# Performance work log

Hardware: AMD Instinct MI355X
Metric: run time of the kernel (lower is better)

Reference implementation:

```python
import jax, jax.numpy as jnp
import numpy as np

DIM = 256
HEADS = 8
WIN = 7          # window height/width
N = WIN * WIN    # tokens per window
HEAD_DIM = DIM // HEADS
CPB_HIDDEN = 512


def _relative_coords_table():
    # [1, 2W-1, 2W-1, 2] log-spaced continuous coords (Swin-V2 CPB input)
    rh = np.arange(-(WIN - 1), WIN, dtype=np.float32)
    rw = np.arange(-(WIN - 1), WIN, dtype=np.float32)
    hh, ww = np.meshgrid(rh, rw, indexing='ij')
    table = np.stack([hh, ww], axis=-1)[None]  # [1, 13, 13, 2]
    table[..., 0] /= (WIN - 1)
    table[..., 1] /= (WIN - 1)
    table *= 8.0
    table = np.sign(table) * np.log(np.abs(table) + 1.0) / np.log(8.0)
    return jnp.asarray(table, dtype=jnp.float32)


def _relative_position_index():
    ch = np.arange(WIN)
    cw = np.arange(WIN)
    coords = np.stack(np.meshgrid(ch, cw, indexing='ij'))  # [2, W, W]
    flat = coords.reshape(2, -1)                            # [2, N]
    rel = flat[:, :, None] - flat[:, None, :]               # [2, N, N]
    rel = rel.transpose(1, 2, 0)
    rel[..., 0] += WIN - 1
    rel[..., 1] += WIN - 1
    rel[..., 0] *= 2 * WIN - 1
    return jnp.asarray(rel.sum(-1), dtype=jnp.int32)        # [N, N]


def setup_inputs() -> dict:
    key = jax.random.key(0)
    ks = jax.random.split(key, 9)
    B = 2048
    s_in = 1.0 / np.sqrt(DIM)
    s_cpb1 = 1.0 / np.sqrt(2.0)
    s_cpb2 = 1.0 / np.sqrt(CPB_HIDDEN)
    return {
        "x": jax.random.normal(ks[0], (B, N, DIM), dtype=jnp.float32),
        "qkv_w": jax.random.normal(ks[1], (DIM, 3 * DIM), dtype=jnp.float32) * s_in,
        "qkv_b": jnp.zeros((3 * DIM,), dtype=jnp.float32),
        "proj_w": jax.random.normal(ks[2], (DIM, DIM), dtype=jnp.float32) * s_in,
        "proj_b": jnp.zeros((DIM,), dtype=jnp.float32),
        "logit_scale": jnp.full((HEADS, 1, 1), np.log(10.0), dtype=jnp.float32),
        "cpb_w1": jax.random.normal(ks[3], (2, CPB_HIDDEN), dtype=jnp.float32) * s_cpb1,
        "cpb_b1": jnp.zeros((CPB_HIDDEN,), dtype=jnp.float32),
        "cpb_w2": jax.random.normal(ks[4], (CPB_HIDDEN, HEADS), dtype=jnp.float32) * s_cpb2,
    }


def reference(x, qkv_w, qkv_b, proj_w, proj_b, logit_scale, cpb_w1, cpb_b1, cpb_w2):
    B = x.shape[0]
    coords_table = _relative_coords_table()       # [1, 13, 13, 2]
    rel_pos_index = _relative_position_index()    # [N, N]

    # QKV projection -> [3, B, H, N, D]
    qkv = (x @ qkv_w + qkv_b).reshape(B, N, 3, HEADS, HEAD_DIM)
    qkv = jnp.transpose(qkv, (2, 0, 3, 1, 4))
    q, k, v = qkv[0], qkv[1], qkv[2]

    # cosine attention: L2-normalize q and k
    qn = q / jnp.linalg.norm(q, axis=-1, keepdims=True)
    kn = k / jnp.linalg.norm(k, axis=-1, keepdims=True)
    attn = jnp.einsum('bhnd,bhmd->bhnm', qn, kn)

    scale = jnp.exp(jnp.clip(logit_scale, -100.0, np.log(1.0 / 0.01)))  # [H,1,1]
    attn = attn * scale[None]

    # CPB-MLP relative position bias
    h = jax.nn.gelu(coords_table @ cpb_w1 + cpb_b1, approximate=False)
    bias_table = (h @ cpb_w2).reshape(-1, HEADS)              # [(2W-1)^2, H]
    bias = bias_table[rel_pos_index.reshape(-1)]              # [N*N, H]
    bias = bias.reshape(N, N, HEADS).transpose(2, 0, 1)       # [H, N, N]
    bias = 16.0 * jax.nn.sigmoid(bias)
    attn = attn + bias[None]

    attn = jax.nn.softmax(attn, axis=-1)

    out = jnp.einsum('bhnm,bhmd->bhnd', attn, v)
    out = jnp.transpose(out, (0, 2, 1, 3)).reshape(B, N, DIM)
    return out @ proj_w + proj_b
```

## Files before the change

kernel.cpp:

```cpp
#include <hip/hip_runtime.h>

typedef _Float16 f16;
typedef _Float16 f16x4 __attribute__((ext_vector_type(4)));
typedef _Float16 f16x8 __attribute__((ext_vector_type(8)));
typedef float f32x4 __attribute__((ext_vector_type(4)));

#define WS_BIAS    0
#define WS_TBL     131072
#define WS_QKVWT   136704
#define WS_PROJWT  529920
#define WS_ATTNOUT 660992

__global__ __launch_bounds__(512) void cpb_mlp_kernel(
    const float* __restrict__ w1, const float* __restrict__ b1,
    const float* __restrict__ w2, float* __restrict__ tbl)
{
    const int bid = blockIdx.x;
    const int i = bid / 13, j = bid % 13;
    float t0 = 8.0f * (float)(i - 6) / 6.0f;
    float t1 = 8.0f * (float)(j - 6) / 6.0f;
    const float invlog8 = 0.4808983469629878f;
    t0 = copysignf(log1pf(fabsf(t0)) * invlog8, t0);
    t1 = copysignf(log1pf(fabsf(t1)) * invlog8, t1);

    const int t = threadIdx.x;
    float pre = t0 * w1[t] + t1 * w1[512 + t] + b1[t];
    float g = 0.5f * pre * (1.0f + erff(pre * 0.70710678118654752f));
    float a[8];
#pragma unroll
    for (int h = 0; h < 8; ++h) a[h] = g * w2[t * 8 + h];
#pragma unroll
    for (int off = 1; off < 64; off <<= 1)
#pragma unroll
        for (int h = 0; h < 8; ++h) a[h] += __shfl_xor(a[h], off, 64);

    __shared__ float wred[8][8];
    const int w = t >> 6, lane = t & 63;
    if (lane == 0)
#pragma unroll
        for (int h = 0; h < 8; ++h) wred[w][h] = a[h];
    __syncthreads();
    if (t < 8) {
        float s = 0.f;
#pragma unroll
        for (int ww = 0; ww < 8; ++ww) s += wred[ww][t];
        tbl[bid * 8 + t] = s;
    }
}

__global__ __launch_bounds__(256) void cpb_bias_kernel(
    const float* __restrict__ tbl, float* __restrict__ bias_ws)
{
    int idx = blockIdx.x * 256 + threadIdx.x;
    int h = idx >> 12, r = (idx >> 6) & 63, c = idx & 63;
    float v = 0.f;
    if (r < 49 && c < 49) {
        int dh = r / 7 - c / 7 + 6;
        int dw = r % 7 - c % 7 + 6;
        float bv = tbl[(dh * 13 + dw) * 8 + h];
        v = 16.0f / (1.0f + __expf(-bv));
    }
    bias_ws[idx] = v;
}

__global__ __launch_bounds__(256) void wconv_kernel(
    const float* __restrict__ qkv_w, const float* __restrict__ proj_w,
    f16* __restrict__ qkv_wT, f16* __restrict__ proj_wT)
{
    __shared__ float ts[64][65];
    int b = blockIdx.x;
    const float* src; f16* dst; int W, kb, nb;
    if (b < 48) { src = qkv_w;  dst = qkv_wT;  W = 768; kb = b / 12; nb = b % 12; }
    else { b -= 48; src = proj_w; dst = proj_wT; W = 256; kb = b / 4;  nb = b % 4; }
    const int t = threadIdx.x;
#pragma unroll
    for (int it = 0; it < 4; ++it) {
        int k = it * 16 + (t >> 4);
        int n4 = (t & 15) * 4;
        float4 v = *(const float4*)(src + (size_t)(kb * 64 + k) * W + nb * 64 + n4);
        ts[k][n4] = v.x; ts[k][n4 + 1] = v.y; ts[k][n4 + 2] = v.z; ts[k][n4 + 3] = v.w;
    }
    __syncthreads();
#pragma unroll
    for (int it = 0; it < 4; ++it) {
        int n = it * 16 + (t >> 4);
        int k4 = (t & 15) * 4;
        f16x4 hv;
        hv[0] = (f16)ts[k4][n]; hv[1] = (f16)ts[k4 + 1][n];
        hv[2] = (f16)ts[k4 + 2][n]; hv[3] = (f16)ts[k4 + 3][n];
        *(f16x4*)(dst + (size_t)(nb * 64 + n) * 256 + kb * 64 + k4) = hv;
    }
}

__global__ __launch_bounds__(256, 3) void win_attn_kernel(
    const float* __restrict__ x, const float* __restrict__ qkv_b,
    const float* __restrict__ logit_scale, const f16* __restrict__ qkv_wT,
    const float* __restrict__ bias_ws, f16* __restrict__ attn_out, int nwg)
{
    __shared__ alignas(16) char smem0[18432];
    __shared__ alignas(16) f16 qs[2][64][40];
    __shared__ alignas(16) f16 kq[2][64][40];
    __shared__ alignas(16) f16 vT[2][32][72];
    __shared__ float invq_s[2][64];
    __shared__ float invk_s[2][64];
    f16 (*xs)[136] = reinterpret_cast<f16(*)[136]>(smem0);
    f16 (*ps)[72]  = reinterpret_cast<f16(*)[72]>(smem0);

    const int orig = blockIdx.x;
    const int wg = ((nwg & 7) == 0) ? ((orig & 7) * (nwg >> 3) + (orig >> 3)) : orig;
    const int b  = wg >> 2;
    const int hp = wg & 3;

    const int tid = threadIdx.x;
    const int lane = tid & 63;
    const int w = tid >> 6;
    const int l15 = lane & 15, lq = lane >> 4;
    const int hl = w >> 1;
    const int dh = w & 1;
    const int head = hp * 2 + hl;

    const float* xb = x + (size_t)b * (49 * 256);
    const int srow = tid >> 5;
    const int scol = (tid & 31) * 4;

    float4 sreg[8];
#pragma unroll
    for (int i = 0; i < 8; ++i) {
        int r = i * 8 + srow;
        sreg[i] = (r < 49) ? *(const float4*)(xb + r * 256 + scol) : make_float4(0.f, 0.f, 0.f, 0.f);
    }
#pragma unroll
    for (int i = 0; i < 8; ++i) {
        int r = i * 8 + srow;
        f16x4 hv; hv[0] = (f16)sreg[i].x; hv[1] = (f16)sreg[i].y; hv[2] = (f16)sreg[i].z; hv[3] = (f16)sreg[i].w;
        *(f16x4*)(&xs[r][scol]) = hv;
    }
    __syncthreads();

#pragma unroll
    for (int i = 0; i < 8; ++i) {
        int r = i * 8 + srow;
        sreg[i] = (r < 49) ? *(const float4*)(xb + r * 256 + 128 + scol) : make_float4(0.f, 0.f, 0.f, 0.f);
    }

    f32x4 acc[3][4];
#pragma unroll
    for (int ci = 0; ci < 3; ++ci)
#pragma unroll
        for (int mt = 0; mt < 4; ++mt) { acc[ci][mt][0] = 0.f; acc[ci][mt][1] = 0.f; acc[ci][mt][2] = 0.f; acc[ci][mt][3] = 0.f; }

    const int bcol = head * 32 + dh * 16 + l15;

#pragma unroll
    for (int ks = 0; ks < 4; ++ks) {
        f16x8 af[4];
#pragma unroll
        for (int mt = 0; mt < 4; ++mt) af[mt] = *(const f16x8*)(&xs[mt * 16 + l15][ks * 32 + lq * 8]);
#pragma unroll
        for (int ci = 0; ci < 3; ++ci) {
            f16x8 bf = *(const f16x8*)(qkv_wT + (size_t)(ci * 256 + bcol) * 256 + ks * 32 + lq * 8);
#pragma unroll
            for (int mt = 0; mt < 4; ++mt)
                acc[ci][mt] = __builtin_amdgcn_mfma_f32_16x16x32_f16(af[mt], bf, acc[ci][mt], 0, 0, 0);
        }
    }
    __syncthreads();

#pragma unroll
    for (int i = 0; i < 8; ++i) {
        int r = i * 8 + srow;
        f16x4 hv; hv[0] = (f16)sreg[i].x; hv[1] = (f16)sreg[i].y; hv[2] = (f16)sreg[i].z; hv[3] = (f16)sreg[i].w;
        *(f16x4*)(&xs[r][scol]) = hv;
    }
    __syncthreads();

#pragma unroll
    for (int ks = 0; ks < 4; ++ks) {
        f16x8 af[4];
#pragma unroll
        for (int mt = 0; mt < 4; ++mt) af[mt] = *(const f16x8*)(&xs[mt * 16 + l15][ks * 32 + lq * 8]);
#pragma unroll
        for (int ci = 0; ci < 3; ++ci) {
            f16x8 bf = *(const f16x8*)(qkv_wT + (size_t)(ci * 256 + bcol) * 256 + 128 + ks * 32 + lq * 8);
#pragma unroll
            for (int mt = 0; mt < 4; ++mt)
                acc[ci][mt] = __builtin_amdgcn_mfma_f32_16x16x32_f16(af[mt], bf, acc[ci][mt], 0, 0, 0);
        }
    }

    {
        float bq = qkv_b[bcol], bk = qkv_b[256 + bcol], bv = qkv_b[512 + bcol];
        const int d = dh * 16 + l15;
#pragma unroll
        for (int mt = 0; mt < 4; ++mt)
#pragma unroll
            for (int j = 0; j < 4; ++j) {
                int row = mt * 16 + lq * 4 + j;
                qs[hl][row][d] = (f16)(acc[0][mt][j] + bq);
                kq[hl][row][d] = (f16)(acc[1][mt][j] + bk);
                vT[hl][d][row] = (f16)(acc[2][mt][j] + bv);
            }
    }
    __syncthreads();

    {
        const int isK = tid >> 7;
        const int h2 = (tid >> 6) & 1;
        const int row = tid & 63;
        const f16* rp = isK ? &kq[h2][row][0] : &qs[h2][row][0];
        float ss = 0.f;
#pragma unroll
        for (int c8 = 0; c8 < 4; ++c8) {
            f16x8 v = *(const f16x8*)(rp + c8 * 8);
#pragma unroll
            for (int e = 0; e < 8; ++e) { float f = (float)v[e]; ss += f * f; }
        }
        float inv = rsqrtf(fmaxf(ss, 1e-20f));
        if (isK) invk_s[h2][row] = inv;
        else {
            float sc = __expf(fminf(logit_scale[hp * 2 + h2], 4.605170185988091f));
            invq_s[h2][row] = inv * sc;
        }
    }
    __syncthreads();

    const int mh = w & 1;
    f32x4 sacc[2][4];
#pragma unroll
    for (int a = 0; a < 2; ++a)
#pragma unroll
        for (int c = 0; c < 4; ++c) { sacc[a][c][0] = 0.f; sacc[a][c][1] = 0.f; sacc[a][c][2] = 0.f; sacc[a][c][3] = 0.f; }
#pragma unroll
    for (int mtl = 0; mtl < 2; ++mtl) {
        int mt = mh * 2 + mtl;
        f16x8 qf = *(const f16x8*)(&qs[hl][mt * 16 + l15][lq * 8]);
#pragma unroll
        for (int nt = 0; nt < 4; ++nt) {
            f16x8 kf = *(const f16x8*)(&kq[hl][nt * 16 + l15][lq * 8]);
            sacc[mtl][nt] = __builtin_amdgcn_mfma_f32_16x16x32_f16(qf, kf, sacc[mtl][nt], 0, 0, 0);
        }
    }

    const float* biash = bias_ws + head * 4096;
#pragma unroll
    for (int mtl = 0; mtl < 2; ++mtl) {
#pragma unroll
        for (int j = 0; j < 4; ++j) {
            int row = (mh * 2 + mtl) * 16 + lq * 4 + j;
            float iq = invq_s[hl][row];
            float tv[4];
#pragma unroll
            for (int nt = 0; nt < 4; ++nt) {
                int col = nt * 16 + l15;
                float sv = sacc[mtl][nt][j] * iq * invk_s[hl][col] + biash[row * 64 + col];
                tv[nt] = (col < 49) ? sv : -1e30f;
            }
            float mx = fmaxf(fmaxf(tv[0], tv[1]), fmaxf(tv[2], tv[3]));
#pragma unroll
            for (int off = 1; off < 16; off <<= 1) mx = fmaxf(mx, __shfl_xor(mx, off, 64));
            float p[4], sum = 0.f;
#pragma unroll
            for (int nt = 0; nt < 4; ++nt) { p[nt] = __expf(tv[nt] - mx); sum += p[nt]; }
#pragma unroll
            for (int off = 1; off < 16; off <<= 1) sum += __shfl_xor(sum, off, 64);
            float invsum = 1.0f / sum;
#pragma unroll
            for (int nt = 0; nt < 4; ++nt) ps[hl * 64 + row][nt * 16 + l15] = (f16)(p[nt] * invsum);
        }
    }

    f32x4 oacc[2][2];
#pragma unroll
    for (int a = 0; a < 2; ++a)
#pragma unroll
        for (int c = 0; c < 2; ++c) { oacc[a][c][0] = 0.f; oacc[a][c][1] = 0.f; oacc[a][c][2] = 0.f; oacc[a][c][3] = 0.f; }
#pragma unroll
    for (int mtl = 0; mtl < 2; ++mtl) {
        int mt = mh * 2 + mtl;
#pragma unroll
        for (int kb = 0; kb < 2; ++kb) {
            f16x8 pf = *(const f16x8*)(&ps[hl * 64 + mt * 16 + l15][kb * 32 + lq * 8]);
#pragma unroll
            for (int nt = 0; nt < 2; ++nt) {
                f16x8 vf = *(const f16x8*)(&vT[hl][nt * 16 + l15][kb * 32 + lq * 8]);
                oacc[mtl][nt] = __builtin_amdgcn_mfma_f32_16x16x32_f16(pf, vf, oacc[mtl][nt], 0, 0, 0);
            }
        }
    }
#pragma unroll
    for (int mtl = 0; mtl < 2; ++mtl)
#pragma unroll
        for (int j = 0; j < 4; ++j) {
            int row = (mh * 2 + mtl) * 16 + lq * 4 + j;
            if (row < 49) {
#pragma unroll
                for (int nt = 0; nt < 2; ++nt)
                    attn_out[((size_t)(b * 49 + row)) * 256 + head * 32 + nt * 16 + l15] = (f16)oacc[mtl][nt][j];
            }
        }
}

__global__ __launch_bounds__(256, 4) void proj_kernel(
    const f16* __restrict__ attn_out, const f16* __restrict__ proj_wT,
    const float* __restrict__ proj_b, float* __restrict__ out, int Mtot)
{
    __shared__ alignas(16) f16 as[64][264];
    const int tid = threadIdx.x, lane = tid & 63, w = tid >> 6;
    const int l15 = lane & 15, lq = lane >> 4;
    const int mb = blockIdx.x;

#pragma unroll
    for (int i = 0; i < 8; ++i) {
        int r = i * 8 + (tid >> 5);
        int c = (tid & 31) * 8;
        int gr = mb * 64 + r;
        f16x8 v = {};
        if (gr < Mtot) v = *(const f16x8*)(attn_out + (size_t)gr * 256 + c);
        *(f16x8*)(&as[r][c]) = v;
    }
    __syncthreads();

    f32x4 acc[4][4];
#pragma unroll
    for (int a = 0; a < 4; ++a)
#pragma unroll
        for (int c = 0; c < 4; ++c) { acc[a][c][0] = 0.f; acc[a][c][1] = 0.f; acc[a][c][2] = 0.f; acc[a][c][3] = 0.f; }

    const f16* bbase = proj_wT + (size_t)(w * 64) * 256;
#pragma unroll
    for (int ks = 0; ks < 8; ++ks) {
        f16x8 af[4], bf[4];
#pragma unroll
        for (int mt = 0; mt < 4; ++mt) af[mt] = *(const f16x8*)(&as[mt * 16 + l15][ks * 32 + lq * 8]);
#pragma unroll
        for (int nt = 0; nt < 4; ++nt) bf[nt] = *(const f16x8*)(bbase + (size_t)(nt * 16 + l15) * 256 + ks * 32 + lq * 8);
#pragma unroll
        for (int mt = 0; mt < 4; ++mt)
#pragma unroll
            for (int nt = 0; nt < 4; ++nt)
                acc[mt][nt] = __builtin_amdgcn_mfma_f32_16x16x32_f16(af[mt], bf[nt], acc[mt][nt], 0, 0, 0);
    }
    float pb[4];
#pragma unroll
    for (int nt = 0; nt < 4; ++nt) pb[nt] = proj_b[w * 64 + nt * 16 + l15];
#pragma unroll
    for (int mt = 0; mt < 4; ++mt)
#pragma unroll
        for (int j = 0; j < 4; ++j) {
            int gr = mb * 64 + mt * 16 + lq * 4 + j;
            if (gr < Mtot) {
#pragma unroll
                for (int nt = 0; nt < 4; ++nt)
                    out[(size_t)gr * 256 + w * 64 + nt * 16 + l15] = acc[mt][nt][j] + pb[nt];
            }
        }
}

extern "C" void kernel_launch(void* const* d_in, const int* in_sizes, int n_in,
                              void* d_out, int out_size, void* d_ws, size_t ws_size,
                              hipStream_t stream) {
    const float* x           = (const float*)d_in[0];
    const float* qkv_w       = (const float*)d_in[1];
    const float* qkv_b       = (const float*)d_in[2];
    const float* proj_w      = (const float*)d_in[3];
    const float* proj_b      = (const float*)d_in[4];
    const float* logit_scale = (const float*)d_in[5];
    const float* cpb_w1      = (const float*)d_in[6];
    const float* cpb_b1      = (const float*)d_in[7];
    const float* cpb_w2      = (const float*)d_in[8];
    float* out = (float*)d_out;

    const int B = in_sizes[0] / (49 * 256);
    char* ws = (char*)d_ws;
    float* bias_ws = (float*)(ws + WS_BIAS);
    float* tbl_ws  = (float*)(ws + WS_TBL);
    f16* qkv_wT    = (f16*)(ws + WS_QKVWT);
    f16* proj_wT   = (f16*)(ws + WS_PROJWT);
    f16* attn_out  = (f16*)(ws + WS_ATTNOUT);

    hipLaunchKernelGGL(cpb_mlp_kernel, dim3(169), dim3(512), 0, stream, cpb_w1, cpb_b1, cpb_w2, tbl_ws);
    hipLaunchKernelGGL(cpb_bias_kernel, dim3(128), dim3(256), 0, stream, tbl_ws, bias_ws);
    hipLaunchKernelGGL(wconv_kernel, dim3(64), dim3(256), 0, stream, qkv_w, proj_w, qkv_wT, proj_wT);

    const int nwg = B * 4;
    hipLaunchKernelGGL(win_attn_kernel, dim3(nwg), dim3(256), 0, stream,
                       x, qkv_b, logit_scale, qkv_wT, bias_ws, attn_out, nwg);

    const int Mtot = B * 49;
    const int mblocks = (Mtot + 63) / 64;
    hipLaunchKernelGGL(proj_kernel, dim3(mblocks), dim3(256), 0, stream,
                       attn_out, proj_wT, proj_b, out, Mtot);
}
```

Baseline: 391.0 us.

## Fuse window attention and output projection into one per-window kernel

Merges the attention and projection kernels so that each 512-thread block handles one whole window with all 8 heads, one wave per head. The per-head attention output stays in LDS and feeds the projection GEMM directly, removing the fp16 intermediate round trip through global memory and one launch. The relative-position bias is stored as fp16 in a permuted layout and held in registers. Q/K norms are computed with in-register shuffles instead of a separate LDS pass, and softmax normalisation is deferred to the output. The cost is higher register and LDS pressure, with occupancy limited to two blocks per CU and fewer blocks overall.

```diff
diff --git a/kernel.cpp b/kernel.cpp
--- a/kernel.cpp
+++ b/kernel.cpp
@@ -6,10 +6,9 @@
 typedef float f32x4 __attribute__((ext_vector_type(4)));
 
 #define WS_BIAS    0
-#define WS_TBL     131072
-#define WS_QKVWT   136704
-#define WS_PROJWT  529920
-#define WS_ATTNOUT 660992
+#define WS_TBL     65536
+#define WS_QKVWT   73728
+#define WS_PROJWT  466944
 
 __global__ __launch_bounds__(512) void cpb_mlp_kernel(
     const float* __restrict__ w1, const float* __restrict__ b1,
@@ -49,7 +48,7 @@
 }
 
 __global__ __launch_bounds__(256) void cpb_bias_kernel(
-    const float* __restrict__ tbl, float* __restrict__ bias_ws)
+    const float* __restrict__ tbl, f16* __restrict__ bias_f16)
 {
     int idx = blockIdx.x * 256 + threadIdx.x;
     int h = idx >> 12, r = (idx >> 6) & 63, c = idx & 63;
@@ -60,7 +59,8 @@
         float bv = tbl[(dh * 13 + dw) * 8 + h];
         v = 16.0f / (1.0f + __expf(-bv));
     }
-    bias_ws[idx] = v;
+    int cc = (c & 15) * 4 + (c >> 4);
+    bias_f16[(h << 12) + (r << 6) + cc] = (f16)v;
 }
 
 __global__ __launch_bounds__(256) void wconv_kernel(
@@ -92,64 +92,67 @@
     }
 }
 
-__global__ __launch_bounds__(256, 3) void win_attn_kernel(
+__global__ __launch_bounds__(512, 2) void fused_kernel(
     const float* __restrict__ x, const float* __restrict__ qkv_b,
     const float* __restrict__ logit_scale, const f16* __restrict__ qkv_wT,
-    const float* __restrict__ bias_ws, f16* __restrict__ attn_out, int nwg)
+    const f16* __restrict__ bias_f16, const f16* __restrict__ proj_wT,
+    const float* __restrict__ proj_b, float* __restrict__ out)
 {
-    __shared__ alignas(16) char smem0[18432];
-    __shared__ alignas(16) f16 qs[2][64][40];
-    __shared__ alignas(16) f16 kq[2][64][40];
-    __shared__ alignas(16) f16 vT[2][32][72];
-    __shared__ float invq_s[2][64];
-    __shared__ float invk_s[2][64];
-    f16 (*xs)[136] = reinterpret_cast<f16(*)[136]>(smem0);
-    f16 (*ps)[72]  = reinterpret_cast<f16(*)[72]>(smem0);
-
-    const int orig = blockIdx.x;
-    const int wg = ((nwg & 7) == 0) ? ((orig & 7) * (nwg >> 3) + (orig >> 3)) : orig;
-    const int b  = wg >> 2;
-    const int hp = wg & 3;
+    __shared__ alignas(16) f16 xs[64][136];
+    __shared__ alignas(16) f16 slab[8 * 5120];
+    __shared__ alignas(16) f16 vt[8][32][72];
+    __shared__ float invk_s[8][64];
 
     const int tid = threadIdx.x;
     const int lane = tid & 63;
-    const int w = tid >> 6;
+    const int head = tid >> 6;
     const int l15 = lane & 15, lq = lane >> 4;
-    const int hl = w >> 1;
-    const int dh = w & 1;
-    const int head = hp * 2 + hl;
+    const int b = blockIdx.x;
+
+    f16x4 bias_r[16];
+    {
+        const f16* bh = bias_f16 + head * 4096;
+#pragma unroll
+        for (int mt = 0; mt < 4; ++mt)
+#pragma unroll
+            for (int j = 0; j < 4; ++j) {
+                int row = mt * 16 + lq * 4 + j;
+                bias_r[mt * 4 + j] = *(const f16x4*)(bh + row * 64 + l15 * 4);
+            }
+    }
+    const float lsc = __expf(fminf(logit_scale[head], 4.605170185988091f));
 
     const float* xb = x + (size_t)b * (49 * 256);
     const int srow = tid >> 5;
     const int scol = (tid & 31) * 4;
 
-    float4 sreg[8];
-#pragma unroll
-    for (int i = 0; i < 8; ++i) {
-        int r = i * 8 + srow;
+    float4 sreg[4];
+#pragma unroll
+    for (int i = 0; i < 4; ++i) {
+        int r = i * 16 + srow;
         sreg[i] = (r < 49) ? *(const float4*)(xb + r * 256 + scol) : make_float4(0.f, 0.f, 0.f, 0.f);
     }
 #pragma unroll
-    for (int i = 0; i < 8; ++i) {
-        int r = i * 8 + srow;
+    for (int i = 0; i < 4; ++i) {
+        int r = i * 16 + srow;
         f16x4 hv; hv[0] = (f16)sreg[i].x; hv[1] = (f16)sreg[i].y; hv[2] = (f16)sreg[i].z; hv[3] = (f16)sreg[i].w;
         *(f16x4*)(&xs[r][scol]) = hv;
     }
     __syncthreads();
 
 #pragma unroll
-    for (int i = 0; i < 8; ++i) {
-        int r = i * 8 + srow;
+    for (int i = 0; i < 4; ++i) {
+        int r = i * 16 + srow;
         sreg[i] = (r < 49) ? *(const float4*)(xb + r * 256 + 128 + scol) : make_float4(0.f, 0.f, 0.f, 0.f);
     }
 
-    f32x4 acc[3][4];
+    f32x4 acc[3][2][4];
 #pragma unroll
     for (int ci = 0; ci < 3; ++ci)
 #pragma unroll
-        for (int mt = 0; mt < 4; ++mt) { acc[ci][mt][0] = 0.f; acc[ci][mt][1] = 0.f; acc[ci][mt][2] = 0.f; acc[ci][mt][3] = 0.f; }
-
-    const int bcol = head * 32 + dh * 16 + l15;
+        for (int nt = 0; nt < 2; ++nt)
+#pragma unroll
+            for (int mt = 0; mt < 4; ++mt) { acc[ci][nt][mt][0]=0.f; acc[ci][nt][mt][1]=0.f; acc[ci][nt][mt][2]=0.f; acc[ci][nt][mt][3]=0.f; }
 
 #pragma unroll
     for (int ks = 0; ks < 4; ++ks) {
@@ -157,18 +160,20 @@
 #pragma unroll
         for (int mt = 0; mt < 4; ++mt) af[mt] = *(const f16x8*)(&xs[mt * 16 + l15][ks * 32 + lq * 8]);
 #pragma unroll
-        for (int ci = 0; ci < 3; ++ci) {
-            f16x8 bf = *(const f16x8*)(qkv_wT + (size_t)(ci * 256 + bcol) * 256 + ks * 32 + lq * 8);
-#pragma unroll
-            for (int mt = 0; mt < 4; ++mt)
-                acc[ci][mt] = __builtin_amdgcn_mfma_f32_16x16x32_f16(af[mt], bf, acc[ci][mt], 0, 0, 0);
-        }
-    }
-    __syncthreads();
-
-#pragma unroll
-    for (int i = 0; i < 8; ++i) {
-        int r = i * 8 + srow;
+        for (int ci = 0; ci < 3; ++ci)
+#pragma unroll
+            for (int nt = 0; nt < 2; ++nt) {
+                f16x8 bf = *(const f16x8*)(qkv_wT + (size_t)(ci * 256 + head * 32 + nt * 16 + l15) * 256 + ks * 32 + lq * 8);
+#pragma unroll
+                for (int mt = 0; mt < 4; ++mt)
+                    acc[ci][nt][mt] = __builtin_amdgcn_mfma_f32_16x16x32_f16(af[mt], bf, acc[ci][nt][mt], 0, 0, 0);
+            }
+    }
+    __syncthreads();
+
+#pragma unroll
+    for (int i = 0; i < 4; ++i) {
+        int r = i * 16 + srow;
         f16x4 hv; hv[0] = (f16)sreg[i].x; hv[1] = (f16)sreg[i].y; hv[2] = (f16)sreg[i].z; hv[3] = (f16)sreg[i].w;
         *(f16x4*)(&xs[r][scol]) = hv;
     }
@@ -180,178 +185,179 @@
 #pragma unroll
         for (int mt = 0; mt < 4; ++mt) af[mt] = *(const f16x8*)(&xs[mt * 16 + l15][ks * 32 + lq * 8]);
 #pragma unroll
-        for (int ci = 0; ci < 3; ++ci) {
-            f16x8 bf = *(const f16x8*)(qkv_wT + (size_t)(ci * 256 + bcol) * 256 + 128 + ks * 32 + lq * 8);
-#pragma unroll
-            for (int mt = 0; mt < 4; ++mt)
-                acc[ci][mt] = __builtin_amdgcn_mfma_f32_16x16x32_f16(af[mt], bf, acc[ci][mt], 0, 0, 0);
-        }
-    }
-
+        for (int ci = 0; ci < 3; ++ci)
+#pragma unroll
+            for (int nt = 0; nt < 2; ++nt) {
+                f16x8 bf = *(const f16x8*)(qkv_wT + (size_t)(ci * 256 + head * 32 + nt * 16 + l15) * 256 + 128 + ks * 32 + lq * 8);
+#pragma unroll
+                for (int mt = 0; mt < 4; ++mt)
+                    acc[ci][nt][mt] = __builtin_amdgcn_mfma_f32_16x16x32_f16(af[mt], bf, acc[ci][nt][mt], 0, 0, 0);
+            }
+    }
+
+    f16* myslab = slab + head * 5120;
+    float bq[2], bk[2], bv2[2];
+#pragma unroll
+    for (int nt = 0; nt < 2; ++nt) {
+        int c = head * 32 + nt * 16 + l15;
+        bq[nt] = qkv_b[c]; bk[nt] = qkv_b[256 + c]; bv2[nt] = qkv_b[512 + c];
+    }
+#pragma unroll
+    for (int nt = 0; nt < 2; ++nt)
+#pragma unroll
+        for (int mt = 0; mt < 4; ++mt)
+#pragma unroll
+            for (int j = 0; j < 4; ++j) {
+                int row = mt * 16 + lq * 4 + j, d = nt * 16 + l15;
+                vt[head][d][row] = (f16)(acc[2][nt][mt][j] + bv2[nt]);
+            }
+    float ssq[4][4], ssk[4][4], invq[4][4], invsum[4][4];
+#pragma unroll
+    for (int mt = 0; mt < 4; ++mt)
+#pragma unroll
+        for (int j = 0; j < 4; ++j) {
+            float sq = 0.f, sk = 0.f;
+            int row = mt * 16 + lq * 4 + j;
+#pragma unroll
+            for (int nt = 0; nt < 2; ++nt) {
+                int d = nt * 16 + l15;
+                float qv = acc[0][nt][mt][j] + bq[nt];
+                float kv = acc[1][nt][mt][j] + bk[nt];
+                myslab[row * 40 + d] = (f16)qv;
+                myslab[2560 + row * 40 + d] = (f16)kv;
+                sq += qv * qv; sk += kv * kv;
+            }
+            ssq[mt][j] = sq; ssk[mt][j] = sk;
+        }
+#pragma unroll
+    for (int off = 1; off < 16; off <<= 1)
+#pragma unroll
+        for (int mt = 0; mt < 4; ++mt)
+#pragma unroll
+            for (int j = 0; j < 4; ++j) {
+                ssq[mt][j] += __shfl_xor(ssq[mt][j], off, 16);
+                ssk[mt][j] += __shfl_xor(ssk[mt][j], off, 16);
+            }
+#pragma unroll
+    for (int mt = 0; mt < 4; ++mt)
+#pragma unroll
+        for (int j = 0; j < 4; ++j) {
+            invq[mt][j] = rsqrtf(fmaxf(ssq[mt][j], 1e-20f)) * lsc;
+            float ik = rsqrtf(fmaxf(ssk[mt][j], 1e-20f));
+            if (l15 == 0) invk_s[head][mt * 16 + lq * 4 + j] = ik;
+        }
+
+    f32x4 sacc[4][4];
+#pragma unroll
+    for (int a = 0; a < 4; ++a)
+#pragma unroll
+        for (int c = 0; c < 4; ++c) { sacc[a][c][0]=0.f; sacc[a][c][1]=0.f; sacc[a][c][2]=0.f; sacc[a][c][3]=0.f; }
     {
-        float bq = qkv_b[bcol], bk = qkv_b[256 + bcol], bv = qkv_b[512 + bcol];
-        const int d = dh * 16 + l15;
+        f16x8 qf[4], kf[4];
+#pragma unroll
+        for (int mt = 0; mt < 4; ++mt) qf[mt] = *(const f16x8*)(myslab + (mt * 16 + l15) * 40 + lq * 8);
+#pragma unroll
+        for (int nt = 0; nt < 4; ++nt) kf[nt] = *(const f16x8*)(myslab + 2560 + (nt * 16 + l15) * 40 + lq * 8);
 #pragma unroll
         for (int mt = 0; mt < 4; ++mt)
 #pragma unroll
-            for (int j = 0; j < 4; ++j) {
-                int row = mt * 16 + lq * 4 + j;
-                qs[hl][row][d] = (f16)(acc[0][mt][j] + bq);
-                kq[hl][row][d] = (f16)(acc[1][mt][j] + bk);
-                vT[hl][d][row] = (f16)(acc[2][mt][j] + bv);
-            }
-    }
-    __syncthreads();
-
-    {
-        const int isK = tid >> 7;
-        const int h2 = (tid >> 6) & 1;
-        const int row = tid & 63;
-        const f16* rp = isK ? &kq[h2][row][0] : &qs[h2][row][0];
-        float ss = 0.f;
-#pragma unroll
-        for (int c8 = 0; c8 < 4; ++c8) {
-            f16x8 v = *(const f16x8*)(rp + c8 * 8);
-#pragma unroll
-            for (int e = 0; e < 8; ++e) { float f = (float)v[e]; ss += f * f; }
-        }
-        float inv = rsqrtf(fmaxf(ss, 1e-20f));
-        if (isK) invk_s[h2][row] = inv;
-        else {
-            float sc = __expf(fminf(logit_scale[hp * 2 + h2], 4.605170185988091f));
-            invq_s[h2][row] = inv * sc;
-        }
-    }
-    __syncthreads();
-
-    const int mh = w & 1;
-    f32x4 sacc[2][4];
-#pragma unroll
-    for (int a = 0; a < 2; ++a)
-#pragma unroll
-        for (int c = 0; c < 4; ++c) { sacc[a][c][0] = 0.f; sacc[a][c][1] = 0.f; sacc[a][c][2] = 0.f; sacc[a][c][3] = 0.f; }
-#pragma unroll
-    for (int mtl = 0; mtl < 2; ++mtl) {
-        int mt = mh * 2 + mtl;
-        f16x8 qf = *(const f16x8*)(&qs[hl][mt * 16 + l15][lq * 8]);
-#pragma unroll
-        for (int nt = 0; nt < 4; ++nt) {
-            f16x8 kf = *(const f16x8*)(&kq[hl][nt * 16 + l15][lq * 8]);
-            sacc[mtl][nt] = __builtin_amdgcn_mfma_f32_16x16x32_f16(qf, kf, sacc[mtl][nt], 0, 0, 0);
-        }
-    }
-
-    const float* biash = bias_ws + head * 4096;
-#pragma unroll
-    for (int mtl = 0; mtl < 2; ++mtl) {
-#pragma unroll
-        for (int j = 0; j < 4; ++j) {
-            int row = (mh * 2 + mtl) * 16 + lq * 4 + j;
-            float iq = invq_s[hl][row];
+            for (int nt = 0; nt < 4; ++nt)
+                sacc[mt][nt] = __builtin_amdgcn_mfma_f32_16x16x32_f16(qf[mt], kf[nt], sacc[mt][nt], 0, 0, 0);
+    }
+
+    float ivk[4];
+#pragma unroll
+    for (int nt = 0; nt < 4; ++nt) ivk[nt] = invk_s[head][nt * 16 + l15];
+#pragma unroll
+    for (int mt = 0; mt < 4; ++mt)
+#pragma unroll
+        for (int j = 0; j < 4; ++j) {
+            float iq = invq[mt][j];
+            f16x4 br = bias_r[mt * 4 + j];
             float tv[4];
 #pragma unroll
             for (int nt = 0; nt < 4; ++nt) {
                 int col = nt * 16 + l15;
-                float sv = sacc[mtl][nt][j] * iq * invk_s[hl][col] + biash[row * 64 + col];
+                float sv = sacc[mt][nt][j] * iq * ivk[nt] + (float)br[nt];
                 tv[nt] = (col < 49) ? sv : -1e30f;
             }
             float mx = fmaxf(fmaxf(tv[0], tv[1]), fmaxf(tv[2], tv[3]));
 #pragma unroll
-            for (int off = 1; off < 16; off <<= 1) mx = fmaxf(mx, __shfl_xor(mx, off, 64));
-            float p[4], sum = 0.f;
-#pragma unroll
-            for (int nt = 0; nt < 4; ++nt) { p[nt] = __expf(tv[nt] - mx); sum += p[nt]; }
-#pragma unroll
-            for (int off = 1; off < 16; off <<= 1) sum += __shfl_xor(sum, off, 64);
-            float invsum = 1.0f / sum;
-#pragma unroll
-            for (int nt = 0; nt < 4; ++nt) ps[hl * 64 + row][nt * 16 + l15] = (f16)(p[nt] * invsum);
-        }
-    }
-
-    f32x4 oacc[2][2];
-#pragma unroll
-    for (int a = 0; a < 2; ++a)
-#pragma unroll
-        for (int c = 0; c < 2; ++c) { oacc[a][c][0] = 0.f; oacc[a][c][1] = 0.f; oacc[a][c][2] = 0.f; oacc[a][c][3] = 0.f; }
-#pragma unroll
-    for (int mtl = 0; mtl < 2; ++mtl) {
-        int mt = mh * 2 + mtl;
-#pragma unroll
-        for (int kb = 0; kb < 2; ++kb) {
-            f16x8 pf = *(const f16x8*)(&ps[hl * 64 + mt * 16 + l15][kb * 32 + lq * 8]);
-#pragma unroll
-            for (int nt = 0; nt < 2; ++nt) {
-                f16x8 vf = *(const f16x8*)(&vT[hl][nt * 16 + l15][kb * 32 + lq * 8]);
-                oacc[mtl][nt] = __builtin_amdgcn_mfma_f32_16x16x32_f16(pf, vf, oacc[mtl][nt], 0, 0, 0);
-            }
-        }
-    }
-#pragma unroll
-    for (int mtl = 0; mtl < 2; ++mtl)
-#pragma unroll
-        for (int j = 0; j < 4; ++j) {
-            int row = (mh * 2 + mtl) * 16 + lq * 4 + j;
+            for (int off = 1; off < 16; off <<= 1) mx = fmaxf(mx, __shfl_xor(mx, off, 16));
+            float p[4], s = 0.f;
+#pragma unroll
+            for (int nt = 0; nt < 4; ++nt) { p[nt] = __expf(tv[nt] - mx); s += p[nt]; }
+            int row = mt * 16 + lq * 4 + j;
+#pragma unroll
+            for (int nt = 0; nt < 4; ++nt) myslab[row * 72 + nt * 16 + l15] = (f16)p[nt];
+#pragma unroll
+            for (int off = 1; off < 16; off <<= 1) s += __shfl_xor(s, off, 16);
+            invsum[mt][j] = 1.0f / s;
+        }
+
+    f32x4 oacc[4][2];
+#pragma unroll
+    for (int a = 0; a < 4; ++a)
+#pragma unroll
+        for (int c = 0; c < 2; ++c) { oacc[a][c][0]=0.f; oacc[a][c][1]=0.f; oacc[a][c][2]=0.f; oacc[a][c][3]=0.f; }
+#pragma unroll
+    for (int kb = 0; kb < 2; ++kb) {
+        f16x8 pf[4];
+#pragma unroll
+        for (int mt = 0; mt < 4; ++mt) pf[mt] = *(const f16x8*)(myslab + (mt * 16 + l15) * 72 + kb * 32 + lq * 8);
+#pragma unroll
+        for (int nt = 0; nt < 2; ++nt) {
+            f16x8 vf = *(const f16x8*)(&vt[head][nt * 16 + l15][kb * 32 + lq * 8]);
+#pragma unroll
+            for (int mt = 0; mt < 4; ++mt)
+                oacc[mt][nt] = __builtin_amdgcn_mfma_f32_16x16x32_f16(pf[mt], vf, oacc[mt][nt], 0, 0, 0);
+        }
+    }
+
+    __syncthreads();
+    f16 (*ao)[264] = reinterpret_cast<f16(*)[264]>(slab);
+#pragma unroll
+    for (int mt = 0; mt < 4; ++mt)
+#pragma unroll
+        for (int j = 0; j < 4; ++j) {
+            int row = mt * 16 + lq * 4 + j;
+#pragma unroll
+            for (int nt = 0; nt < 2; ++nt)
+                ao[row][head * 32 + nt * 16 + l15] = (f16)(oacc[mt][nt][j] * invsum[mt][j]);
+        }
+    __syncthreads();
+
+    f32x4 pacc[4][2];
+#pragma unroll
+    for (int a = 0; a < 4; ++a)
+#pragma unroll
+        for (int c = 0; c < 2; ++c) { pacc[a][c][0]=0.f; pacc[a][c][1]=0.f; pacc[a][c][2]=0.f; pacc[a][c][3]=0.f; }
+#pragma unroll
+    for (int ks = 0; ks < 8; ++ks) {
+        f16x8 af2[4];
+#pragma unroll
+        for (int mt = 0; mt < 4; ++mt) af2[mt] = *(const f16x8*)(&ao[mt * 16 + l15][ks * 32 + lq * 8]);
+#pragma unroll
+        for (int nt = 0; nt < 2; ++nt) {
+            f16x8 bf = *(const f16x8*)(proj_wT + (size_t)(head * 32 + nt * 16 + l15) * 256 + ks * 32 + lq * 8);
+#pragma unroll
+            for (int mt = 0; mt < 4; ++mt)
+                pacc[mt][nt] = __builtin_amdgcn_mfma_f32_16x16x32_f16(af2[mt], bf, pacc[mt][nt], 0, 0, 0);
+        }
+    }
+    float pb[2];
+#pragma unroll
+    for (int nt = 0; nt < 2; ++nt) pb[nt] = proj_b[head * 32 + nt * 16 + l15];
+#pragma unroll
+    for (int mt = 0; mt < 4; ++mt)
+#pragma unroll
+        for (int j = 0; j < 4; ++j) {
+            int row = mt * 16 + lq * 4 + j;
             if (row < 49) {
+                float* orow = out + ((size_t)(b * 49 + row)) * 256 + head * 32;
 #pragma unroll
                 for (int nt = 0; nt < 2; ++nt)
-                    attn_out[((size_t)(b * 49 + row)) * 256 + head * 32 + nt * 16 + l15] = (f16)oacc[mtl][nt][j];
-            }
-        }
-}
-
-__global__ __launch_bounds__(256, 4) void proj_kernel(
-    const f16* __restrict__ attn_out, const f16* __restrict__ proj_wT,
-    const float* __restrict__ proj_b, float* __restrict__ out, int Mtot)
-{
-    __shared__ alignas(16) f16 as[64][264];
-    const int tid = threadIdx.x, lane = tid & 63, w = tid >> 6;
-    const int l15 = lane & 15, lq = lane >> 4;
-    const int mb = blockIdx.x;
-
-#pragma unroll
-    for (int i = 0; i < 8; ++i) {
-        int r = i * 8 + (tid >> 5);
-        int c = (tid & 31) * 8;
-        int gr = mb * 64 + r;
-        f16x8 v = {};
-        if (gr < Mtot) v = *(const f16x8*)(attn_out + (size_t)gr * 256 + c);
-        *(f16x8*)(&as[r][c]) = v;
-    }
-    __syncthreads();
-
-    f32x4 acc[4][4];
-#pragma unroll
-    for (int a = 0; a < 4; ++a)
-#pragma unroll
-        for (int c = 0; c < 4; ++c) { acc[a][c][0] = 0.f; acc[a][c][1] = 0.f; acc[a][c][2] = 0.f; acc[a][c][3] = 0.f; }
-
-    const f16* bbase = proj_wT + (size_t)(w * 64) * 256;
-#pragma unroll
-    for (int ks = 0; ks < 8; ++ks) {
-        f16x8 af[4], bf[4];
-#pragma unroll
-        for (int mt = 0; mt < 4; ++mt) af[mt] = *(const f16x8*)(&as[mt * 16 + l15][ks * 32 + lq * 8]);
-#pragma unroll
-        for (int nt = 0; nt < 4; ++nt) bf[nt] = *(const f16x8*)(bbase + (size_t)(nt * 16 + l15) * 256 + ks * 32 + lq * 8);
-#pragma unroll
-        for (int mt = 0; mt < 4; ++mt)
-#pragma unroll
-            for (int nt = 0; nt < 4; ++nt)
-                acc[mt][nt] = __builtin_amdgcn_mfma_f32_16x16x32_f16(af[mt], bf[nt], acc[mt][nt], 0, 0, 0);
-    }
-    float pb[4];
-#pragma unroll
-    for (int nt = 0; nt < 4; ++nt) pb[nt] = proj_b[w * 64 + nt * 16 + l15];
-#pragma unroll
-    for (int mt = 0; mt < 4; ++mt)
-#pragma unroll
-        for (int j = 0; j < 4; ++j) {
-            int gr = mb * 64 + mt * 16 + lq * 4 + j;
-            if (gr < Mtot) {
-#pragma unroll
-                for (int nt = 0; nt < 4; ++nt)
-                    out[(size_t)gr * 256 + w * 64 + nt * 16 + l15] = acc[mt][nt][j] + pb[nt];
+                    orow[nt * 16 + l15] = pacc[mt][nt][j] + pb[nt];
             }
         }
 }
@@ -372,22 +378,14 @@
 
     const int B = in_sizes[0] / (49 * 256);
     char* ws = (char*)d_ws;
-    float* bias_ws = (float*)(ws + WS_BIAS);
-    float* tbl_ws  = (float*)(ws + WS_TBL);
-    f16* qkv_wT    = (f16*)(ws + WS_QKVWT);
-    f16* proj_wT   = (f16*)(ws + WS_PROJWT);
-    f16* attn_out  = (f16*)(ws + WS_ATTNOUT);
+    f16* bias_f16 = (f16*)(ws + WS_BIAS);
+    float* tbl_ws = (float*)(ws + WS_TBL);
+    f16* qkv_wT   = (f16*)(ws + WS_QKVWT);
+    f16* proj_wT  = (f16*)(ws + WS_PROJWT);
 
     hipLaunchKernelGGL(cpb_mlp_kernel, dim3(169), dim3(512), 0, stream, cpb_w1, cpb_b1, cpb_w2, tbl_ws);
-    hipLaunchKernelGGL(cpb_bias_kernel, dim3(128), dim3(256), 0, stream, tbl_ws, bias_ws);
+    hipLaunchKernelGGL(cpb_bias_kernel, dim3(128), dim3(256), 0, stream, tbl_ws, bias_f16);
     hipLaunchKernelGGL(wconv_kernel, dim3(64), dim3(256), 0, stream, qkv_w, proj_w, qkv_wT, proj_wT);
-
-    const int nwg = B * 4;
-    hipLaunchKernelGGL(win_attn_kernel, dim3(nwg), dim3(256), 0, stream,
-                       x, qkv_b, logit_scale, qkv_wT, bias_ws, attn_out, nwg);
-
-    const int Mtot = B * 49;
-    const int mblocks = (Mtot + 63) / 64;
-    hipLaunchKernelGGL(proj_kernel, dim3(mblocks), dim3(256), 0, stream,
-                       attn_out, proj_wT, proj_b, out, Mtot);
-}
+    hipLaunchKernelGGL(fused_kernel, dim3(B), dim3(512), 0, stream,
+                       x, qkv_b, logit_scale, qkv_wT, bias_f16, proj_wT, proj_b, out);
+}
```

Result: slower. 408.7 us (+4.5%).
